# Performance work log

Measured on AMD Instinct MI355X. Metric: run time of the kernel, lower is better.

Reference implementation:

```python
import jax, jax.numpy as jnp
import numpy as np

N = 256
MAX_LENGTH = 1024
BATCH = 256


def _legs_transition(n):
    # HiPPO-LegS transition: A[i,j] = -sqrt(2i+1)sqrt(2j+1) (i>j), -(i+1) (i==j), 0 else
    q = np.arange(n, dtype=np.float64)
    col, row = np.meshgrid(q, q)
    r = 2 * q + 1
    M = -(np.where(row >= col, r, 0) - np.diag(q))
    T = np.sqrt(np.diag(2 * q + 1))
    A = T @ M @ np.linalg.inv(T)
    B = np.diag(T)  # B squeezed to (N,)
    return A, B


def _discretize_bilinear(n, L):
    A, B = _legs_transition(n)
    I = np.eye(n)
    A_st = np.empty((L, n, n), dtype=np.float64)
    B_st = np.empty((L, n), dtype=np.float64)
    for t in range(1, L + 1):  # setup-time only, not traced
        At = A / t
        lhs = I - At / 2.0  # lower triangular, invertible
        A_st[t - 1] = np.linalg.solve(lhs, I + At / 2.0)
        B_st[t - 1] = np.linalg.solve(lhs, B / t)
    return A_st.astype(np.float32), B_st.astype(np.float32)


def setup_inputs() -> dict:
    key = jax.random.key(0)
    inputs = jax.random.normal(key, (MAX_LENGTH, BATCH), dtype=jnp.float32)
    A_st, B_st = _discretize_bilinear(N, MAX_LENGTH)
    return {
        "inputs": inputs,
        "A_stacked": jnp.asarray(A_st),  # (L, N, N)
        "B_stacked": jnp.asarray(B_st),  # (L, N)
    }


def reference(inputs, A_stacked, B_stacked):
    # inputs: (L, B) -> output (L, B, N)
    L, Bdim = inputs.shape
    n = A_stacked.shape[-1]
    # u_t[b, :] = B_t * inputs[t, b]
    u = inputs[..., None] * B_stacked[:L][:, None, :]  # (L, B, N)

    def step(x, inp):
        A_t, u_t = inp  # (N, N), (B, N)
        x = u_t + x @ A_t.T  # x_t = A_t x_{t-1} + B_t u_t
        return x, x

    x0 = jnp.zeros((Bdim, n), dtype=inputs.dtype)
    _, ys = jax.lax.scan(step, x0, (A_stacked[:L], u))
    return ys  # (L, B, N)
```

## Files before the change

kernel.cpp:

```cpp
#include <hip/hip_runtime.h>


typedef float f32x4 __attribute__((ext_vector_type(4)));

#define LSTEPS   1024
#define BATCH    256
#define NDIM     256
#define NWG      256
#define THREADS  1024
#define H0C      6208
#define H1C      2112
#define H0SLOTS  97
#define H1SLOTS  33
#define H0ISS    7
#define H1ISS    3
#define XSOFF    ((H0C + H1C) * 4)
#define SMEM_BYTES ((XSOFF + 2 * NDIM) * 4)

__device__ __forceinline__ int rs0(int r) {
    if (r >= 128) return 2112 + (r - 128) * 32;
    int q = r >> 2;
    return 2 * q * (q - 1) + (r - (q << 2)) * q + r;
}
__device__ __forceinline__ int rs1(int r) {
    int q = r >> 2;
    int S = 2 * q * (q - 1) + (r - (q << 2)) * q;
    return S - 1984 - 31 * (r - 128);
}
__device__ __forceinline__ int frow0(int c) {
    int lo = 0, hi = 255;
    while (lo < hi) { int mid = (lo + hi + 1) >> 1; if (rs0(mid) <= c) lo = mid; else hi = mid - 1; }
    return lo;
}
__device__ __forceinline__ int frow1(int c) {
    int lo = 128, hi = 255;
    while (lo < hi) { int mid = (lo + hi + 1) >> 1; if (rs1(mid) <= c) lo = mid; else hi = mid - 1; }
    return lo;
}
__device__ __forceinline__ void gload_lds16(const float* g, float* l) {
    __builtin_amdgcn_global_load_lds(
        (const __attribute__((address_space(1))) void*)g,
        (__attribute__((address_space(3))) void*)l, 16, 0, 0);
}

__global__ __launch_bounds__(THREADS)
void hippo_scan(const float* __restrict__ inp,
                const float* __restrict__ A,
                const float* __restrict__ Bst,
                float* __restrict__ out)
{
    extern __shared__ float smem[];
    float* Ab = smem;

    const int T    = threadIdx.x;
    const int lane = T & 63;
    const int wave = T >> 6;
    const int g    = T >> 4;
    const int s    = T & 15;
    const int b    = blockIdx.x;

    int rows[4] = {2 * g, 2 * g + 1, 254 - 2 * g, 255 - 2 * g};
    const int sel0 = s & 1, sel1 = (s >> 1) & 1;
    const int rowOwn = rows[sel0 + 2 * sel1];
    const bool writer = (s < 4);

    int a0base[4], mmax[4];
#pragma unroll
    for (int i = 0; i < 4; ++i) { a0base[i] = rs0(rows[i]) * 4; mmax[i] = rows[i] >> 2; }
    int a1base[2];
    a1base[0] = (H0C + rs1(rows[2]) - 32) * 4;
    a1base[1] = (H0C + rs1(rows[3]) - 32) * 4;

    int gsrc0[H0ISS], lbase0[H0ISS];
#pragma unroll
    for (int p = 0; p < H0ISS; ++p) {
        int slot = wave + 16 * p; if (slot >= H0SLOTS) slot -= 16;
        int c = slot * 64 + lane;
        int r = frow0(c);
        gsrc0[p]  = r * NDIM + (c - rs0(r)) * 4;
        lbase0[p] = slot * 256;
    }
    int gsrc1[H1ISS], lbase1[H1ISS];
#pragma unroll
    for (int p = 0; p < H1ISS; ++p) {
        int slot = wave + 16 * p; if (slot >= H1SLOTS) slot -= 16;
        int c = slot * 64 + lane;
        int r = frow1(c);
        gsrc1[p]  = r * NDIM + 128 + (c - rs1(r)) * 4;
        lbase1[p] = H0C * 4 + slot * 256;
    }

    if (T < 2 * NDIM) smem[XSOFF + T] = 0.f;

    {
        const float* As = A;
#pragma unroll
        for (int p = 0; p < H0ISS; ++p) gload_lds16(As + gsrc0[p], Ab + lbase0[p]);
#pragma unroll
        for (int p = 0; p < H1ISS; ++p) gload_lds16(As + gsrc1[p], Ab + lbase1[p]);
    }
    asm volatile("s_waitcnt vmcnt(0) lgkmcnt(0)" ::: "memory");
    __builtin_amdgcn_s_barrier();

    for (int t = 0; t < LSTEPS; ++t) {
        float* xc = smem + XSOFF + ((t & 1) ? NDIM : 0);
        float* xn = smem + XSOFF + ((t & 1) ? 0 : NDIM);
        const float* As = A + (size_t)((t + 1 < LSTEPS) ? t + 1 : t) * (NDIM * NDIM);

        const f32x4 xv0 = *(const f32x4*)&xc[s * 4];
        const f32x4 xv1 = *(const f32x4*)&xc[64 + s * 4];

        float acc[4] = {0.f, 0.f, 0.f, 0.f};
#pragma unroll
        for (int i = 0; i < 4; ++i) {
            if (s <= mmax[i]) {
                const f32x4 a = *(const f32x4*)&Ab[a0base[i] + s * 4];
                acc[i] = fmaf(a[0], xv0[0], acc[i]);
                acc[i] = fmaf(a[1], xv0[1], acc[i]);
                acc[i] = fmaf(a[2], xv0[2], acc[i]);
                acc[i] = fmaf(a[3], xv0[3], acc[i]);
            }
        }
#pragma unroll
        for (int i = 0; i < 4; ++i) {
            if (16 + s <= mmax[i]) {
                const f32x4 a = *(const f32x4*)&Ab[a0base[i] + (16 + s) * 4];
                acc[i] = fmaf(a[0], xv1[0], acc[i]);
                acc[i] = fmaf(a[1], xv1[1], acc[i]);
                acc[i] = fmaf(a[2], xv1[2], acc[i]);
                acc[i] = fmaf(a[3], xv1[3], acc[i]);
            }
        }

        asm volatile("s_waitcnt vmcnt(0)" ::: "memory");
        asm volatile("s_waitcnt lgkmcnt(0)" ::: "memory");
        __builtin_amdgcn_s_barrier();

#pragma unroll
        for (int p = 0; p < H0ISS; ++p) gload_lds16(As + gsrc0[p], Ab + lbase0[p]);

        const float scal_in = inp[t * BATCH + b];
        const float scal_b  = Bst[t * NDIM + rowOwn];
        if (t > 0 && lane < 16)
            out[(size_t)(t - 1) * (BATCH * NDIM) + (size_t)b * NDIM + wave * 16 + lane]
                = xc[wave * 16 + lane];

        const f32x4 xv2 = *(const f32x4*)&xc[128 + s * 4];
        const f32x4 xv3 = *(const f32x4*)&xc[192 + s * 4];

#pragma unroll
        for (int i = 2; i < 4; ++i) {
            if (32 + s <= mmax[i]) {
                const f32x4 a = *(const f32x4*)&Ab[a1base[i - 2] + (32 + s) * 4];
                acc[i] = fmaf(a[0], xv2[0], acc[i]);
                acc[i] = fmaf(a[1], xv2[1], acc[i]);
                acc[i] = fmaf(a[2], xv2[2], acc[i]);
                acc[i] = fmaf(a[3], xv2[3], acc[i]);
            }
            if (48 + s <= mmax[i]) {
                const f32x4 a = *(const f32x4*)&Ab[a1base[i - 2] + (48 + s) * 4];
                acc[i] = fmaf(a[0], xv3[0], acc[i]);
                acc[i] = fmaf(a[1], xv3[1], acc[i]);
                acc[i] = fmaf(a[2], xv3[2], acc[i]);
                acc[i] = fmaf(a[3], xv3[3], acc[i]);
            }
        }

        asm volatile("s_waitcnt lgkmcnt(0)" ::: "memory");
        __builtin_amdgcn_s_barrier();
#pragma unroll
        for (int p = 0; p < H1ISS; ++p) gload_lds16(As + gsrc1[p], Ab + lbase1[p]);

        const float c0 = (sel0 ? acc[1] : acc[0]) + __shfl_xor(sel0 ? acc[0] : acc[1], 1);
        const float c1 = (sel0 ? acc[3] : acc[2]) + __shfl_xor(sel0 ? acc[2] : acc[3], 1);
        float d = (sel1 ? c1 : c0) + __shfl_xor(sel1 ? c0 : c1, 2);
        d += __shfl_xor(d, 4);
        d += __shfl_xor(d, 8);
        const float v = fmaf(scal_in, scal_b, d);
        if (writer) xn[rowOwn] = v;

        asm volatile("s_waitcnt vmcnt(3)" ::: "memory");
        asm volatile("s_waitcnt lgkmcnt(0)" ::: "memory");
        __builtin_amdgcn_s_barrier();
    }

    if (lane < 16)
        out[(size_t)(LSTEPS - 1) * (BATCH * NDIM) + (size_t)b * NDIM + wave * 16 + lane]
            = smem[XSOFF + wave * 16 + lane];
}

extern "C" void kernel_launch(void* const* d_in, const int* in_sizes, int n_in,
                              void* d_out, int out_size, void* d_ws, size_t ws_size,
                              hipStream_t stream) {
    const float* inp = (const float*)d_in[0];
    const float* A   = (const float*)d_in[1];
    const float* Bst = (const float*)d_in[2];
    float* out = (float*)d_out;
    (void)hipFuncSetAttribute((const void*)hippo_scan,
                              hipFuncAttributeMaxDynamicSharedMemorySize, SMEM_BYTES);
    hipLaunchKernelGGL(hippo_scan, dim3(NWG), dim3(THREADS), SMEM_BYTES, stream,
                       inp, A, Bst, out);
}
```

Measured before the change: 3.378 ms.

## Process two batch rows per workgroup to reuse each streamed A tile

Each workgroup now handles two batch columns, so it runs on 128 workgroups instead of 256. Every A_t tile streamed from global memory into LDS is reused for two state vectors, which halves total A traffic across the GPU. The shuffle reduction is reorganised so lanes split by batch index, and the state buffers are padded to 260 floats. In exchange there is less parallelism (half the workgroups on a device with more CUs than that) and twice the FMA and LDS read work per step inside each workgroup.

```diff
diff --git a/kernel.cpp b/kernel.cpp
--- a/kernel.cpp
+++ b/kernel.cpp
@@ -6,7 +6,8 @@
 #define LSTEPS   1024
 #define BATCH    256
 #define NDIM     256
-#define NWG      256
+#define NWG      128
+#define BB       2
 #define THREADS  1024
 #define H0C      6208
 #define H1C      2112
@@ -14,8 +15,9 @@
 #define H1SLOTS  33
 #define H0ISS    7
 #define H1ISS    3
+#define XPL      260
 #define XSOFF    ((H0C + H1C) * 4)
-#define SMEM_BYTES ((XSOFF + 2 * NDIM) * 4)
+#define SMEMB    ((XSOFF + 2 * BB * XPL) * 4)
 
 __device__ __forceinline__ int rs0(int r) {
     if (r >= 128) return 2112 + (r - 128) * 32;
@@ -57,12 +59,14 @@
     const int wave = T >> 6;
     const int g    = T >> 4;
     const int s    = T & 15;
-    const int b    = blockIdx.x;
+    const int b0   = blockIdx.x * BB;
 
     int rows[4] = {2 * g, 2 * g + 1, 254 - 2 * g, 255 - 2 * g};
-    const int sel0 = s & 1, sel1 = (s >> 1) & 1;
-    const int rowOwn = rows[sel0 + 2 * sel1];
-    const bool writer = (s < 4);
+    const int bOwn = s & 1;
+    const int sel1 = (s >> 1) & 1;
+    const int sel2 = (s >> 2) & 1;
+    const int rowOwn = rows[sel1 + 2 * sel2];
+    const bool writer = (s < 8);
 
     int a0base[4], mmax[4];
 #pragma unroll
@@ -90,45 +94,55 @@
         lbase1[p] = H0C * 4 + slot * 256;
     }
 
-    if (T < 2 * NDIM) smem[XSOFF + T] = 0.f;
-
-    {
-        const float* As = A;
-#pragma unroll
-        for (int p = 0; p < H0ISS; ++p) gload_lds16(As + gsrc0[p], Ab + lbase0[p]);
-#pragma unroll
-        for (int p = 0; p < H1ISS; ++p) gload_lds16(As + gsrc1[p], Ab + lbase1[p]);
-    }
+    for (int i = T; i < 2 * BB * XPL; i += THREADS) smem[XSOFF + i] = 0.f;
+
+#pragma unroll
+    for (int p = 0; p < H0ISS; ++p) gload_lds16(A + gsrc0[p], Ab + lbase0[p]);
+#pragma unroll
+    for (int p = 0; p < H1ISS; ++p) gload_lds16(A + gsrc1[p], Ab + lbase1[p]);
     asm volatile("s_waitcnt vmcnt(0) lgkmcnt(0)" ::: "memory");
     __builtin_amdgcn_s_barrier();
 
     for (int t = 0; t < LSTEPS; ++t) {
-        float* xc = smem + XSOFF + ((t & 1) ? NDIM : 0);
-        float* xn = smem + XSOFF + ((t & 1) ? 0 : NDIM);
+        float* xc = smem + XSOFF + ((t & 1) ? BB * XPL : 0);
+        float* xn = smem + XSOFF + ((t & 1) ? 0 : BB * XPL);
         const float* As = A + (size_t)((t + 1 < LSTEPS) ? t + 1 : t) * (NDIM * NDIM);
 
-        const f32x4 xv0 = *(const f32x4*)&xc[s * 4];
-        const f32x4 xv1 = *(const f32x4*)&xc[64 + s * 4];
-
-        float acc[4] = {0.f, 0.f, 0.f, 0.f};
+        const f32x4 xva0 = *(const f32x4*)&xc[s * 4];
+        const f32x4 xvb0 = *(const f32x4*)&xc[64 + s * 4];
+        const f32x4 xva1 = *(const f32x4*)&xc[XPL + s * 4];
+        const f32x4 xvb1 = *(const f32x4*)&xc[XPL + 64 + s * 4];
+
+        float acc[4][BB];
+#pragma unroll
+        for (int i = 0; i < 4; ++i) { acc[i][0] = 0.f; acc[i][1] = 0.f; }
+
 #pragma unroll
         for (int i = 0; i < 4; ++i) {
             if (s <= mmax[i]) {
                 const f32x4 a = *(const f32x4*)&Ab[a0base[i] + s * 4];
-                acc[i] = fmaf(a[0], xv0[0], acc[i]);
-                acc[i] = fmaf(a[1], xv0[1], acc[i]);
-                acc[i] = fmaf(a[2], xv0[2], acc[i]);
-                acc[i] = fmaf(a[3], xv0[3], acc[i]);
+                acc[i][0] = fmaf(a[0], xva0[0], acc[i][0]);
+                acc[i][0] = fmaf(a[1], xva0[1], acc[i][0]);
+                acc[i][0] = fmaf(a[2], xva0[2], acc[i][0]);
+                acc[i][0] = fmaf(a[3], xva0[3], acc[i][0]);
+                acc[i][1] = fmaf(a[0], xva1[0], acc[i][1]);
+                acc[i][1] = fmaf(a[1], xva1[1], acc[i][1]);
+                acc[i][1] = fmaf(a[2], xva1[2], acc[i][1]);
+                acc[i][1] = fmaf(a[3], xva1[3], acc[i][1]);
             }
         }
 #pragma unroll
         for (int i = 0; i < 4; ++i) {
             if (16 + s <= mmax[i]) {
                 const f32x4 a = *(const f32x4*)&Ab[a0base[i] + (16 + s) * 4];
-                acc[i] = fmaf(a[0], xv1[0], acc[i]);
-                acc[i] = fmaf(a[1], xv1[1], acc[i]);
-                acc[i] = fmaf(a[2], xv1[2], acc[i]);
-                acc[i] = fmaf(a[3], xv1[3], acc[i]);
+                acc[i][0] = fmaf(a[0], xvb0[0], acc[i][0]);
+                acc[i][0] = fmaf(a[1], xvb0[1], acc[i][0]);
+                acc[i][0] = fmaf(a[2], xvb0[2], acc[i][0]);
+                acc[i][0] = fmaf(a[3], xvb0[3], acc[i][0]);
+                acc[i][1] = fmaf(a[0], xvb1[0], acc[i][1]);
+                acc[i][1] = fmaf(a[1], xvb1[1], acc[i][1]);
+                acc[i][1] = fmaf(a[2], xvb1[2], acc[i][1]);
+                acc[i][1] = fmaf(a[3], xvb1[3], acc[i][1]);
             }
         }
 
@@ -139,30 +153,42 @@
 #pragma unroll
         for (int p = 0; p < H0ISS; ++p) gload_lds16(As + gsrc0[p], Ab + lbase0[p]);
 
-        const float scal_in = inp[t * BATCH + b];
+        const float scal_in = inp[t * BATCH + b0 + bOwn];
         const float scal_b  = Bst[t * NDIM + rowOwn];
-        if (t > 0 && lane < 16)
-            out[(size_t)(t - 1) * (BATCH * NDIM) + (size_t)b * NDIM + wave * 16 + lane]
-                = xc[wave * 16 + lane];
-
-        const f32x4 xv2 = *(const f32x4*)&xc[128 + s * 4];
-        const f32x4 xv3 = *(const f32x4*)&xc[192 + s * 4];
+        if (t > 0 && lane < 32) {
+            const int bi = lane >> 4, col = wave * 16 + (lane & 15);
+            out[(size_t)(t - 1) * (BATCH * NDIM) + (size_t)(b0 + bi) * NDIM + col]
+                = xc[bi * XPL + col];
+        }
+
+        const f32x4 xvc0 = *(const f32x4*)&xc[128 + s * 4];
+        const f32x4 xvd0 = *(const f32x4*)&xc[192 + s * 4];
+        const f32x4 xvc1 = *(const f32x4*)&xc[XPL + 128 + s * 4];
+        const f32x4 xvd1 = *(const f32x4*)&xc[XPL + 192 + s * 4];
 
 #pragma unroll
         for (int i = 2; i < 4; ++i) {
             if (32 + s <= mmax[i]) {
                 const f32x4 a = *(const f32x4*)&Ab[a1base[i - 2] + (32 + s) * 4];
-                acc[i] = fmaf(a[0], xv2[0], acc[i]);
-                acc[i] = fmaf(a[1], xv2[1], acc[i]);
-                acc[i] = fmaf(a[2], xv2[2], acc[i]);
-                acc[i] = fmaf(a[3], xv2[3], acc[i]);
+                acc[i][0] = fmaf(a[0], xvc0[0], acc[i][0]);
+                acc[i][0] = fmaf(a[1], xvc0[1], acc[i][0]);
+                acc[i][0] = fmaf(a[2], xvc0[2], acc[i][0]);
+                acc[i][0] = fmaf(a[3], xvc0[3], acc[i][0]);
+                acc[i][1] = fmaf(a[0], xvc1[0], acc[i][1]);
+                acc[i][1] = fmaf(a[1], xvc1[1], acc[i][1]);
+                acc[i][1] = fmaf(a[2], xvc1[2], acc[i][1]);
+                acc[i][1] = fmaf(a[3], xvc1[3], acc[i][1]);
             }
             if (48 + s <= mmax[i]) {
                 const f32x4 a = *(const f32x4*)&Ab[a1base[i - 2] + (48 + s) * 4];
-                acc[i] = fmaf(a[0], xv3[0], acc[i]);
-                acc[i] = fmaf(a[1], xv3[1], acc[i]);
-                acc[i] = fmaf(a[2], xv3[2], acc[i]);
-                acc[i] = fmaf(a[3], xv3[3], acc[i]);
+                acc[i][0] = fmaf(a[0], xvd0[0], acc[i][0]);
+                acc[i][0] = fmaf(a[1], xvd0[1], acc[i][0]);
+                acc[i][0] = fmaf(a[2], xvd0[2], acc[i][0]);
+                acc[i][0] = fmaf(a[3], xvd0[3], acc[i][0]);
+                acc[i][1] = fmaf(a[0], xvd1[0], acc[i][1]);
+                acc[i][1] = fmaf(a[1], xvd1[1], acc[i][1]);
+                acc[i][1] = fmaf(a[2], xvd1[2], acc[i][1]);
+                acc[i][1] = fmaf(a[3], xvd1[3], acc[i][1]);
             }
         }
 
@@ -171,22 +197,37 @@
 #pragma unroll
         for (int p = 0; p < H1ISS; ++p) gload_lds16(As + gsrc1[p], Ab + lbase1[p]);
 
-        const float c0 = (sel0 ? acc[1] : acc[0]) + __shfl_xor(sel0 ? acc[0] : acc[1], 1);
-        const float c1 = (sel0 ? acc[3] : acc[2]) + __shfl_xor(sel0 ? acc[2] : acc[3], 1);
-        float d = (sel1 ? c1 : c0) + __shfl_xor(sel1 ? c0 : c1, 2);
-        d += __shfl_xor(d, 4);
-        d += __shfl_xor(d, 8);
-        const float v = fmaf(scal_in, scal_b, d);
-        if (writer) xn[rowOwn] = v;
+        float c[4];
+#pragma unroll
+        for (int i = 0; i < 4; ++i) {
+            const float keep = bOwn ? acc[i][1] : acc[i][0];
+            const float send = bOwn ? acc[i][0] : acc[i][1];
+            c[i] = keep + __shfl_xor(send, 1);
+        }
+        float d[2];
+#pragma unroll
+        for (int m = 0; m < 2; ++m) {
+            const float keep = c[2 * m + sel1];
+            const float send = c[2 * m + (1 - sel1)];
+            d[m] = keep + __shfl_xor(send, 2);
+        }
+        const float e = d[sel2] + __shfl_xor(d[1 - sel2], 4);
+        float v = e + __shfl_xor(e, 8);
+
+        v = fmaf(scal_in, scal_b, v);
+        if (writer) xn[bOwn * XPL + rowOwn] = v;
 
         asm volatile("s_waitcnt vmcnt(3)" ::: "memory");
         asm volatile("s_waitcnt lgkmcnt(0)" ::: "memory");
         __builtin_amdgcn_s_barrier();
     }
 
-    if (lane < 16)
-        out[(size_t)(LSTEPS - 1) * (BATCH * NDIM) + (size_t)b * NDIM + wave * 16 + lane]
-            = smem[XSOFF + wave * 16 + lane];
+    if (lane < 32) {
+        const int bi = lane >> 4, col = wave * 16 + (lane & 15);
+        out[(size_t)(LSTEPS - 1) * (BATCH * NDIM) + (size_t)(b0 + bi) * NDIM + col]
+            = smem[XSOFF + bi * XPL + col];
+    }
+    asm volatile("s_waitcnt vmcnt(0)" ::: "memory");
 }
 
 extern "C" void kernel_launch(void* const* d_in, const int* in_sizes, int n_in,
@@ -197,7 +238,7 @@
     const float* Bst = (const float*)d_in[2];
     float* out = (float*)d_out;
     (void)hipFuncSetAttribute((const void*)hippo_scan,
-                              hipFuncAttributeMaxDynamicSharedMemorySize, SMEM_BYTES);
-    hipLaunchKernelGGL(hippo_scan, dim3(NWG), dim3(THREADS), SMEM_BYTES, stream,
+                              hipFuncAttributeMaxDynamicSharedMemorySize, SMEMB);
+    hipLaunchKernelGGL(hippo_scan, dim3(NWG), dim3(THREADS), SMEMB, stream,
                        inp, A, Bst, out);
 }
```

Result: slower. 3.461 ms (+2.5%).
